# Kernel optimization log

Measured on AMD Instinct MI355X. Metric: run time of the kernel, lower is better.

## Reference

```python
import jax, jax.numpy as jnp
import numpy as np

N = 20000      # total nodes
E = 160000     # total edges
G = 64         # graphs in batch
D_ESM = 1280
D = 512
OUT = 500
NUM_LAYERS = 3


def setup_inputs() -> dict:
    key = jax.random.key(0)
    ks = jax.random.split(key, 16)
    s = 0.02
    inp = {
        "native_x": jax.random.randint(ks[0], (N,), 0, 21),
        "x": jax.random.normal(ks[1], (N, D_ESM), dtype=jnp.float32),
        "edge_index": jax.random.randint(ks[2], (2, E), 0, N),
        "batch": jnp.sort(jax.random.randint(ks[3], (N,), 0, G)),
        # parameters
        "embed_table": jax.random.normal(ks[4], (21, 96), dtype=jnp.float32) * s,
        "proj_aa_w": jax.random.normal(ks[5], (96, D), dtype=jnp.float32) * s,
        "proj_aa_b": jnp.zeros((D,), jnp.float32),
        "proj_esm_w": jax.random.normal(ks[6], (D_ESM, D), dtype=jnp.float32) * s,
        "proj_esm_b": jnp.zeros((D,), jnp.float32),
        "gcn_w": jax.random.normal(ks[7], (NUM_LAYERS, D, D), dtype=jnp.float32) * s,
        "gcn_b": jnp.zeros((NUM_LAYERS, D), jnp.float32),
        "ro1_w": jax.random.normal(ks[8], (D, 1024), dtype=jnp.float32) * s,
        "ro1_b": jnp.zeros((1024,), jnp.float32),
        "ro2_w": jax.random.normal(ks[9], (1024, OUT), dtype=jnp.float32) * s,
        "ro2_b": jnp.zeros((OUT,), jnp.float32),
        "weight1": jnp.array([0.6, 0.4], jnp.float32),
    }
    return inp


def _gcn_stack(feat, src, dst, enorm, self_norm, gcn_w, gcn_b):
    # GraphCNN: 3 GCNConv layers (PyG: sym-normalized adj with self loops),
    # residual add after the first layer.
    for i in range(NUM_LAYERS):
        hW = feat @ gcn_w[i]                                   # [N, D]
        msg = hW[src] * enorm[:, None]                          # [E, D] gather
        agg = jax.ops.segment_sum(msg, dst, num_segments=N)     # scatter-add
        agg = agg + hW * self_norm[:, None] + gcn_b[i]
        out = jax.nn.relu(agg)
        feat = out if i == 0 else feat + out
    return feat


def reference(native_x, x, edge_index, batch, embed_table,
              proj_aa_w, proj_aa_b, proj_esm_w, proj_esm_b,
              gcn_w, gcn_b, ro1_w, ro1_b, ro2_w, ro2_b, weight1):
    # embedding + projections (dropout = identity, eval mode)
    x_aa = embed_table[native_x] @ proj_aa_w + proj_aa_b        # [N, 512]
    x_esm_lin = x @ proj_esm_w + proj_esm_b                     # [N, 512]
    h = jax.nn.relu(x_aa + x_esm_lin)
    x_esm = jax.nn.relu(x_esm_lin)

    src, dst = edge_index[0], edge_index[1]
    # GCN normalization with self loops: deg over targets + 1
    deg = jax.ops.segment_sum(jnp.ones((E,), x.dtype), dst, num_segments=N) + 1.0
    dis = deg ** -0.5
    enorm = dis[src] * dis[dst]     # per-edge norm
    self_norm = dis * dis           # self-loop norm

    n1 = _gcn_stack(h, src, dst, enorm, self_norm, gcn_w, gcn_b)
    n3 = _gcn_stack(x_esm, src, dst, enorm, self_norm, gcn_w, gcn_b)

    # global max pool per graph
    g1 = jax.ops.segment_max(n1, batch, num_segments=G)          # [G, 512]
    g3 = jax.ops.segment_max(n3, batch, num_segments=G)

    g = weight1[0] * g1 + weight1[1] * g3
    y = jax.nn.sigmoid(jax.nn.relu(g @ ro1_w + ro1_b) @ ro2_w + ro2_b)
    return y
```

## Files before the change

### kernel.cpp

```cpp
#include <hip/hip_runtime.h>
#include <float.h>

#define NN 20000
#define EE 160000
#define GG 64
#define DD 512
#define NL 3
#define M2 40000
#define M2P 40064
#define M1 20000
#define M1P 20096
#define BK 64

typedef __bf16 bf16x8 __attribute__((ext_vector_type(8)));
typedef float f32x4 __attribute__((ext_vector_type(4)));
typedef unsigned int u32;
typedef unsigned short u16;
typedef u32 u32x4 __attribute__((ext_vector_type(4)));
typedef u32 u32x2 __attribute__((ext_vector_type(2)));

union FragU { u32x4 u; bf16x8 b; };

__device__ inline float blo(u32 u){ union{u32 i;float f;}x; x.i=u<<16; return x.f; }
__device__ inline float bhi(u32 u){ union{u32 i;float f;}x; x.i=u&0xFFFF0000u; return x.f; }
__device__ inline float bf2f(u16 v){ union{u32 i;float f;}x; x.i=((u32)v)<<16; return x.f; }
__device__ inline u16 f2bf(float f){ union{float f;u32 i;}x; x.f=f; u32 r=x.i+0x7FFFu+((x.i>>16)&1u); return (u16)(r>>16); }
__device__ inline u32 pack2(float a,float b){ return (u32)f2bf(a) | ((u32)f2bf(b)<<16); }

__device__ __forceinline__ void gload16(const void* g, void* lds){
  __builtin_amdgcn_global_load_lds(
    (const __attribute__((address_space(1))) void*)g,
    (__attribute__((address_space(3))) void*)lds, 16, 0, 0);
}

__global__ void k_cvt(const float* __restrict__ in, u16* __restrict__ outp){
  int t = blockIdx.x*256+threadIdx.x;
  if(t >= M1P*160) return;
  int row = t/160, gidx = t%160;
  u32x4 o;
  if(row < M1){
    const float* s = in + (size_t)row*1280 + gidx*8;
    float4 v0 = *(const float4*)s;
    float4 v1 = *(const float4*)(s+4);
    o.x=pack2(v0.x,v0.y); o.y=pack2(v0.z,v0.w);
    o.z=pack2(v1.x,v1.y); o.w=pack2(v1.z,v1.w);
  } else {
    o.x=o.y=o.z=o.w=0u;
  }
  *(u32x4*)(outp + (size_t)row*1280 + gidx*8) = o;
}

__global__ void k_transpose_cvt(const float* __restrict__ in, u16* __restrict__ outp, int R, int C){
  __shared__ float t[32][33];
  int c0 = blockIdx.x*32, r0 = blockIdx.y*32;
  t[threadIdx.y][threadIdx.x] = in[(size_t)(r0+threadIdx.y)*C + c0+threadIdx.x];
  __syncthreads();
  outp[(size_t)(c0+threadIdx.y)*R + r0+threadIdx.x] = f2bf(t[threadIdx.x][threadIdx.y]);
}

__global__ void k_transpose_f32(const float* __restrict__ in, float* __restrict__ outp, int R, int C){
  __shared__ float t[32][33];
  int c0 = blockIdx.x*32, r0 = blockIdx.y*32;
  int r = r0+threadIdx.y, c = c0+threadIdx.x;
  if(r<R && c<C) t[threadIdx.y][threadIdx.x] = in[(size_t)r*C + c];
  __syncthreads();
  int oc = c0+threadIdx.y, orr = r0+threadIdx.x;
  if(oc<C && orr<R) outp[(size_t)oc*R + orr] = t[threadIdx.x][threadIdx.y];
}

__global__ void k_embp(const float* __restrict__ et, const float* __restrict__ w,
                       const float* __restrict__ b, float* __restrict__ outp){
  int t = blockIdx.x*256+threadIdx.x;
  if(t >= 21*512) return;
  int a = t>>9, d = t&511;
  float s = b[d];
  for(int k=0;k<96;k++) s += et[a*96+k]*w[k*512+d];
  outp[t] = s;
}

__global__ void k_deg(const int* __restrict__ ei, int* __restrict__ deg){
  int e = blockIdx.x*256+threadIdx.x; if(e>=EE) return;
  atomicAdd(&deg[ei[EE+e]], 1);
}
__global__ void k_dis(const int* __restrict__ deg, float* __restrict__ dis){
  int n = blockIdx.x*256+threadIdx.x; if(n>=NN) return;
  dis[n] = rsqrtf((float)deg[n] + 1.0f);
}
__global__ void k_scan(const int* __restrict__ deg, int* __restrict__ offs){
  __shared__ int part[1024];
  int tid = threadIdx.x;
  int base = tid*20;
  int s=0;
  for(int i=0;i<20;i++){ int idx=base+i; if(idx<NN) s += deg[idx]; }
  part[tid]=s; __syncthreads();
  for(int off=1; off<1024; off<<=1){
    int v = (tid>=off)? part[tid-off] : 0;
    __syncthreads();
    part[tid] += v;
    __syncthreads();
  }
  int pre = (tid>0)? part[tid-1] : 0;
  for(int i=0;i<20;i++){ int idx=base+i; if(idx<NN){ offs[idx]=pre; pre += deg[idx]; } }
  if(tid==1023) offs[NN]=part[1023];
}
__global__ void k_fill(const int* __restrict__ ei, const int* __restrict__ offs, int* __restrict__ curs,
                       const float* __restrict__ dis, int* __restrict__ csrs, float* __restrict__ csrw){
  int e = blockIdx.x*256+threadIdx.x; if(e>=EE) return;
  int s = ei[e], d = ei[EE+e];
  int pos = atomicAdd(&curs[d],1);
  int slot = offs[d]+pos;
  csrs[slot]=s;
  csrw[slot]=dis[s]*dis[d];
}

__global__ __launch_bounds__(256) void k_gemm(const u16* __restrict__ A, const u16* __restrict__ Bt,
                                              u16* __restrict__ C, int Mstore, int K, int lda){
  __shared__ u16 lsA[128*BK];
  __shared__ u16 lsB[128*BK];
  const int tid = threadIdx.x;
  const int lane = tid & 63;
  const int wid = tid >> 6;
  const int wr = wid >> 1, wc = wid & 1;
  const int la = lane & 15, lg = lane >> 4;
  const int n0 = blockIdx.x * 128;
  const int rowB = blockIdx.y * 128;

  f32x4 acc[4][4];
  #pragma unroll
  for(int m=0;m<4;m++)
    #pragma unroll
    for(int n=0;n<4;n++)
      #pragma unroll
      for(int r=0;r<4;r++) acc[m][n][r]=0.f;

  const u16* Arow = A + (size_t)rowB*lda;
  const u16* Brow = Bt + (size_t)n0*K;

  int srow[4], scol[4], ldsoff[4];
  #pragma unroll
  for(int i=0;i<4;i++){
    int li = i*256+tid;
    srow[i] = li>>3;
    scol[i] = ((li&7) ^ (srow[i]&7))*8;
    ldsoff[i] = (i*256 + wid*64)*8;
  }

  for(int k0=0;k0<K;k0+=BK){
    #pragma unroll
    for(int i=0;i<4;i++)
      gload16(Arow + (size_t)srow[i]*lda + k0 + scol[i], lsA + ldsoff[i]);
    #pragma unroll
    for(int i=0;i<4;i++)
      gload16(Brow + (size_t)srow[i]*K + k0 + scol[i], lsB + ldsoff[i]);
    __syncthreads();
    #pragma unroll
    for(int kk=0;kk<2;kk++){
      FragU aF[4], bF[4];
      #pragma unroll
      for(int m=0;m<4;m++){
        int row = wr*64+m*16+la;
        aF[m].u = *(const u32x4*)&lsA[row*BK + ((kk*4+lg)^(row&7))*8];
      }
      #pragma unroll
      for(int n=0;n<4;n++){
        int row = wc*64+n*16+la;
        bF[n].u = *(const u32x4*)&lsB[row*BK + ((kk*4+lg)^(row&7))*8];
      }
      #pragma unroll
      for(int m=0;m<4;m++)
        #pragma unroll
        for(int n=0;n<4;n++)
          acc[m][n] = __builtin_amdgcn_mfma_f32_16x16x32_bf16(aF[m].b, bF[n].b, acc[m][n], 0,0,0);
    }
    __syncthreads();
  }
  #pragma unroll
  for(int m=0;m<4;m++)
    #pragma unroll
    for(int n=0;n<4;n++)
      #pragma unroll
      for(int r=0;r<4;r++){
        int rr = rowB + wr*64 + m*16 + lg*4 + r;
        if(rr < Mstore)
          C[(size_t)rr*512 + n0 + wc*64 + n*16 + la] = f2bf(acc[m][n][r]);
      }
}

__global__ void k_fuse(const u16* __restrict__ xW, const int* __restrict__ nx,
                       const float* __restrict__ embp, const float* __restrict__ esm_b,
                       u16* __restrict__ feat){
  int t = blockIdx.x*256+threadIdx.x;
  if(t >= NN*64) return;
  int n = t>>6, c = (t&63)*8;
  uint4 q = *(const uint4*)(xW + (size_t)n*512 + c);
  int a = nx[n];
  float xw[8] = {blo(q.x),bhi(q.x),blo(q.y),bhi(q.y),blo(q.z),bhi(q.z),blo(q.w),bhi(q.w)};
  float h[8], ee[8];
  #pragma unroll
  for(int j=0;j<8;j++){
    float t1 = xw[j] + esm_b[c+j];
    float hh = embp[a*512 + c + j] + t1;
    h[j]  = hh>0.f?hh:0.f;
    ee[j] = t1>0.f?t1:0.f;
  }
  uint4 o1, o2;
  o1.x=pack2(h[0],h[1]); o1.y=pack2(h[2],h[3]); o1.z=pack2(h[4],h[5]); o1.w=pack2(h[6],h[7]);
  o2.x=pack2(ee[0],ee[1]); o2.y=pack2(ee[2],ee[3]); o2.z=pack2(ee[4],ee[5]); o2.w=pack2(ee[6],ee[7]);
  *(uint4*)(feat + (size_t)n*512 + c) = o1;
  *(uint4*)(feat + (size_t)(n+NN)*512 + c) = o2;
}

__global__ __launch_bounds__(64) void k_agg(const u16* __restrict__ hW, u16* __restrict__ feat,
                 const int* __restrict__ offs, const int* __restrict__ csrs,
                 const float* __restrict__ csrw, const float* __restrict__ dis,
                 const float* __restrict__ bias, int layer){
  const int v = blockIdx.x;
  const int lane = threadIdx.x;
  const int nn  = (v < NN) ? v : v - NN;
  const int soff = (v < NN) ? 0 : NN;
  const int e0 = offs[nn], e1 = offs[nn+1];
  float acc[8] = {0,0,0,0,0,0,0,0};
  for(int e=e0;e<e1;++e){
    int s = csrs[e] + soff;
    float wgt = csrw[e];
    uint4 q = *(const uint4*)(hW + (size_t)s*512 + lane*8);
    acc[0]+=wgt*blo(q.x); acc[1]+=wgt*bhi(q.x);
    acc[2]+=wgt*blo(q.y); acc[3]+=wgt*bhi(q.y);
    acc[4]+=wgt*blo(q.z); acc[5]+=wgt*bhi(q.z);
    acc[6]+=wgt*blo(q.w); acc[7]+=wgt*bhi(q.w);
  }
  float dn = dis[nn]; float sn = dn*dn;
  uint4 qs = *(const uint4*)(hW + (size_t)v*512 + lane*8);
  acc[0]+=sn*blo(qs.x); acc[1]+=sn*bhi(qs.x); acc[2]+=sn*blo(qs.y); acc[3]+=sn*bhi(qs.y);
  acc[4]+=sn*blo(qs.z); acc[5]+=sn*bhi(qs.z); acc[6]+=sn*blo(qs.w); acc[7]+=sn*bhi(qs.w);
  float4 b0 = *(const float4*)(bias + lane*8);
  float4 b1 = *(const float4*)(bias + lane*8 + 4);
  acc[0]+=b0.x; acc[1]+=b0.y; acc[2]+=b0.z; acc[3]+=b0.w;
  acc[4]+=b1.x; acc[5]+=b1.y; acc[6]+=b1.z; acc[7]+=b1.w;
  #pragma unroll
  for(int j=0;j<8;j++) acc[j] = acc[j]>0.f ? acc[j] : 0.f;
  if(layer>0){
    uint4 qf = *(const uint4*)(feat + (size_t)v*512 + lane*8);
    acc[0]+=blo(qf.x); acc[1]+=bhi(qf.x); acc[2]+=blo(qf.y); acc[3]+=bhi(qf.y);
    acc[4]+=blo(qf.z); acc[5]+=bhi(qf.z); acc[6]+=blo(qf.w); acc[7]+=bhi(qf.w);
  }
  uint4 o;
  o.x=pack2(acc[0],acc[1]); o.y=pack2(acc[2],acc[3]);
  o.z=pack2(acc[4],acc[5]); o.w=pack2(acc[6],acc[7]);
  *(uint4*)(feat + (size_t)v*512 + lane*8) = o;
}

__global__ void k_bounds(const int* __restrict__ batch, int* __restrict__ starts){
  int n = blockIdx.x*256+threadIdx.x;
  if(n>=NN) return;
  int b = batch[n];
  int pb = n ? batch[n-1] : -1;
  for(int g=pb+1; g<=b; g++) starts[g]=n;
  if(n==NN-1){ for(int g=b+1; g<=GG; g++) starts[g]=NN; }
}

__global__ void k_pool(const u16* __restrict__ feat, const int* __restrict__ starts,
                       u32* __restrict__ m1, u32* __restrict__ m3){
  int g = blockIdx.x, c = blockIdx.y;
  int s = starts[g], e = starts[g+1];
  int len = e - s;
  int b0 = s + (len*c)/8, b1 = s + (len*(c+1))/8;
  int t = threadIdx.x;
  float a0=0.f, a1=0.f, c0=0.f, c1=0.f;
  for(int n=b0;n<b1;++n){
    u32 q1 = *(const u32*)(feat + (size_t)n*512 + t*2);
    u32 q3 = *(const u32*)(feat + (size_t)(n+NN)*512 + t*2);
    a0 = fmaxf(a0, blo(q1)); a1 = fmaxf(a1, bhi(q1));
    c0 = fmaxf(c0, blo(q3)); c1 = fmaxf(c1, bhi(q3));
  }
  atomicMax(m1 + g*512 + t*2,     __float_as_uint(a0));
  atomicMax(m1 + g*512 + t*2 + 1, __float_as_uint(a1));
  atomicMax(m3 + g*512 + t*2,     __float_as_uint(c0));
  atomicMax(m3 + g*512 + t*2 + 1, __float_as_uint(c1));
}
__global__ void k_gcomb(const u32* __restrict__ m1, const u32* __restrict__ m3,
                        const float* __restrict__ w1, float* __restrict__ gc){
  int t = blockIdx.x*256+threadIdx.x; if(t>=GG*512) return;
  gc[t] = w1[0]*__uint_as_float(m1[t]) + w1[1]*__uint_as_float(m3[t]);
}

__global__ __launch_bounds__(256) void k_ro1v(const float* __restrict__ gc, const float* __restrict__ wT,
                                              const float* __restrict__ b, float* __restrict__ r1){
  int gw = blockIdx.x*4 + (threadIdx.x>>6);
  int g = gw >> 10, o = gw & 1023;
  int lane = threadIdx.x & 63;
  const float4* gr = (const float4*)(gc + (size_t)g*512);
  const float4* wr = (const float4*)(wT + (size_t)o*512);
  float s = 0.f;
  #pragma unroll
  for(int i=0;i<2;i++){
    float4 a = gr[i*64+lane];
    float4 w = wr[i*64+lane];
    s += a.x*w.x + a.y*w.y + a.z*w.z + a.w*w.w;
  }
  #pragma unroll
  for(int m=32;m>=1;m>>=1) s += __shfl_xor(s, m, 64);
  if(lane==0){ s += b[o]; r1[gw] = s>0.f ? s : 0.f; }
}
__global__ __launch_bounds__(256) void k_ro2v(const float* __restrict__ r1, const float* __restrict__ wT,
                                              const float* __restrict__ b, float* __restrict__ y){
  int gw = blockIdx.x*4 + (threadIdx.x>>6);
  int g = gw/500, o = gw - g*500;
  int lane = threadIdx.x & 63;
  const float4* gr = (const float4*)(r1 + (size_t)g*1024);
  const float4* wr = (const float4*)(wT + (size_t)o*1024);
  float s = 0.f;
  #pragma unroll
  for(int i=0;i<4;i++){
    float4 a = gr[i*64+lane];
    float4 w = wr[i*64+lane];
    s += a.x*w.x + a.y*w.y + a.z*w.z + a.w*w.w;
  }
  #pragma unroll
  for(int m=32;m>=1;m>>=1) s += __shfl_xor(s, m, 64);
  if(lane==0) y[gw] = 1.0f/(1.0f+__expf(-(s + b[o])));
}

extern "C" void kernel_launch(void* const* d_in, const int* in_sizes, int n_in,
                              void* d_out, int out_size, void* d_ws, size_t ws_size,
                              hipStream_t stream){
  const int*   native_x = (const int*)d_in[0];
  const float* x        = (const float*)d_in[1];
  const int*   ei       = (const int*)d_in[2];
  const int*   batch    = (const int*)d_in[3];
  const float* embed_t  = (const float*)d_in[4];
  const float* paa_w    = (const float*)d_in[5];
  const float* paa_b    = (const float*)d_in[6];
  const float* pesm_w   = (const float*)d_in[7];
  const float* pesm_b   = (const float*)d_in[8];
  const float* gcn_w    = (const float*)d_in[9];
  const float* gcn_b    = (const float*)d_in[10];
  const float* ro1_w    = (const float*)d_in[11];
  const float* ro1_b    = (const float*)d_in[12];
  const float* ro2_w    = (const float*)d_in[13];
  const float* ro2_b    = (const float*)d_in[14];
  const float* w1       = (const float*)d_in[15];
  float* out = (float*)d_out;

  char* p = (char*)d_ws;
  auto alloc = [&](size_t n){ void* r = (void*)p; p += (n + 255) & ~(size_t)255; return r; };
  u16* feat   = (u16*)alloc((size_t)M2P*512*2);
  u16* hW     = (u16*)alloc((size_t)M2P*512*2);
  u16* xbf    = (u16*)alloc((size_t)M1P*1280*2);
  u16* WtE    = (u16*)alloc((size_t)512*1280*2);
  u16* WtG    = (u16*)alloc((size_t)3*512*512*2);
  float* roT1 = (float*)alloc((size_t)1024*512*4);
  float* roT2 = (float*)alloc((size_t)500*1024*4);
  float* embp = (float*)alloc(21*512*4);
  int* deg    = (int*)alloc(NN*4);
  float* dis  = (float*)alloc(NN*4);
  int* offs   = (int*)alloc((NN+1)*4);
  int* curs   = (int*)alloc(NN*4);
  int* csrs   = (int*)alloc(EE*4);
  float* csrw = (float*)alloc(EE*4);
  int* starts = (int*)alloc((GG+1)*4);
  u32* m1b    = (u32*)alloc(GG*512*4);
  u32* m3b    = (u32*)alloc(GG*512*4);
  float* gc   = (float*)alloc(GG*512*4);
  float* r1   = (float*)alloc(GG*1024*4);
  (void)ws_size; (void)in_sizes; (void)n_in; (void)out_size;

  hipMemsetAsync(deg,  0, NN*4, stream);
  hipMemsetAsync(curs, 0, NN*4, stream);
  hipMemsetAsync(m1b,  0, GG*512*4, stream);
  hipMemsetAsync(m3b,  0, GG*512*4, stream);

  k_cvt<<<(M1P*160+255)/256,256,0,stream>>>(x, xbf);
  k_transpose_cvt<<<dim3(16,40),dim3(32,32),0,stream>>>(pesm_w, WtE, 1280, 512);
  for(int i=0;i<3;i++)
    k_transpose_cvt<<<dim3(16,16),dim3(32,32),0,stream>>>(gcn_w+(size_t)i*262144, WtG+(size_t)i*262144, 512, 512);
  k_transpose_f32<<<dim3(32,16),dim3(32,32),0,stream>>>(ro1_w, roT1, 512, 1024);
  k_transpose_f32<<<dim3(16,32),dim3(32,32),0,stream>>>(ro2_w, roT2, 1024, 500);
  k_embp<<<42,256,0,stream>>>(embed_t, paa_w, paa_b, embp);
  k_deg<<<(EE+255)/256,256,0,stream>>>(ei, deg);
  k_dis<<<(NN+255)/256,256,0,stream>>>(deg, dis);
  k_scan<<<1,1024,0,stream>>>(deg, offs);
  k_fill<<<(EE+255)/256,256,0,stream>>>(ei, offs, curs, dis, csrs, csrw);

  k_gemm<<<dim3(4,157),256,0,stream>>>(xbf, WtE, hW, M1, 1280, 1280);
  k_fuse<<<(NN*64+255)/256,256,0,stream>>>(hW, native_x, embp, pesm_b, feat);

  for(int i=0;i<3;i++){
    k_gemm<<<dim3(4,313),256,0,stream>>>(feat, WtG+(size_t)i*262144, hW, M2, 512, 512);
    k_agg<<<M2,64,0,stream>>>(hW, feat, offs, csrs, csrw, dis, gcn_b+(size_t)i*512, i);
  }

  k_bounds<<<(NN+255)/256,256,0,stream>>>(batch, starts);
  k_pool<<<dim3(GG,8),256,0,stream>>>(feat, starts, m1b, m3b);
  k_gcomb<<<(GG*512+255)/256,256,0,stream>>>(m1b, m3b, w1, gc);
  k_ro1v<<<16384,256,0,stream>>>(gc, roT1, ro1_b, r1);
  k_ro2v<<<8000,256,0,stream>>>(r1, roT2, ro2_b, out);
}
```

Baseline: 481.7 us.

## Interleave the two GCN stacks row-wise and split aggregation across edge-parallel lanes

Node features for the two GCN stacks are stored interleaved, as rows 2n and 2n+1, instead of as two separate halves. A neighbour gather therefore fetches both stacks' rows for a source node from adjacent memory, and the CSR index and weight are shared between the two streams. The aggregation kernel becomes a 256-thread block in which each wave handles one node and a 64-column slice, with 4 lane groups walking edges in parallel and combining through cross-lane shuffles. The aim is to shorten the serial, latency-bound per-edge loop and raise memory-level parallelism. The cost is redundant edge-metadata loads across the 8 column slices and the shuffle-reduction overhead.

```diff
diff --git a/kernel.cpp b/kernel.cpp
--- a/kernel.cpp
+++ b/kernel.cpp
@@ -31,6 +31,13 @@
   __builtin_amdgcn_global_load_lds(
     (const __attribute__((address_space(1))) void*)g,
     (__attribute__((address_space(3))) void*)lds, 16, 0, 0);
+}
+
+__device__ __forceinline__ void acc8(float* a, uint4 q, float w){
+  a[0]+=w*blo(q.x); a[1]+=w*bhi(q.x);
+  a[2]+=w*blo(q.y); a[3]+=w*bhi(q.y);
+  a[4]+=w*blo(q.z); a[5]+=w*bhi(q.z);
+  a[6]+=w*blo(q.w); a[7]+=w*bhi(q.w);
 }
 
 __global__ void k_cvt(const float* __restrict__ in, u16* __restrict__ outp){
@@ -206,48 +213,64 @@
   uint4 o1, o2;
   o1.x=pack2(h[0],h[1]); o1.y=pack2(h[2],h[3]); o1.z=pack2(h[4],h[5]); o1.w=pack2(h[6],h[7]);
   o2.x=pack2(ee[0],ee[1]); o2.y=pack2(ee[2],ee[3]); o2.z=pack2(ee[4],ee[5]); o2.w=pack2(ee[6],ee[7]);
-  *(uint4*)(feat + (size_t)n*512 + c) = o1;
-  *(uint4*)(feat + (size_t)(n+NN)*512 + c) = o2;
-}
-
-__global__ __launch_bounds__(64) void k_agg(const u16* __restrict__ hW, u16* __restrict__ feat,
+  *(uint4*)(feat + (size_t)(2*n)*512 + c) = o1;
+  *(uint4*)(feat + (size_t)(2*n+1)*512 + c) = o2;
+}
+
+__global__ __launch_bounds__(256) void k_agg3(const u16* __restrict__ hW, u16* __restrict__ feat,
                  const int* __restrict__ offs, const int* __restrict__ csrs,
                  const float* __restrict__ csrw, const float* __restrict__ dis,
                  const float* __restrict__ bias, int layer){
-  const int v = blockIdx.x;
-  const int lane = threadIdx.x;
-  const int nn  = (v < NN) ? v : v - NN;
-  const int soff = (v < NN) ? 0 : NN;
+  const int tid = threadIdx.x;
+  const int wv = tid >> 6;
+  const int lane = tid & 63;
+  const int slice = blockIdx.x & 7;
+  const int nn = ((blockIdx.x >> 3) << 2) + wv;
+  const int g = lane >> 4;
+  const int p = lane & 15;
+  const int st = p >> 3;
+  const int ch = p & 7;
+  const int eo = slice*64 + ch*8;
+
   const int e0 = offs[nn], e1 = offs[nn+1];
   float acc[8] = {0,0,0,0,0,0,0,0};
-  for(int e=e0;e<e1;++e){
-    int s = csrs[e] + soff;
-    float wgt = csrw[e];
-    uint4 q = *(const uint4*)(hW + (size_t)s*512 + lane*8);
-    acc[0]+=wgt*blo(q.x); acc[1]+=wgt*bhi(q.x);
-    acc[2]+=wgt*blo(q.y); acc[3]+=wgt*bhi(q.y);
-    acc[4]+=wgt*blo(q.z); acc[5]+=wgt*bhi(q.z);
-    acc[6]+=wgt*blo(q.w); acc[7]+=wgt*bhi(q.w);
-  }
-  float dn = dis[nn]; float sn = dn*dn;
-  uint4 qs = *(const uint4*)(hW + (size_t)v*512 + lane*8);
-  acc[0]+=sn*blo(qs.x); acc[1]+=sn*bhi(qs.x); acc[2]+=sn*blo(qs.y); acc[3]+=sn*bhi(qs.y);
-  acc[4]+=sn*blo(qs.z); acc[5]+=sn*bhi(qs.z); acc[6]+=sn*blo(qs.w); acc[7]+=sn*bhi(qs.w);
-  float4 b0 = *(const float4*)(bias + lane*8);
-  float4 b1 = *(const float4*)(bias + lane*8 + 4);
+
+  uint4 qs = *(const uint4*)(hW + (size_t)(2*nn+st)*512 + eo);
+  float dn = dis[nn], sn = dn*dn;
+
+  for(int eb = e0; eb < e1; eb += 4){
+    int e = eb + g;
+    uint4 q = make_uint4(0u,0u,0u,0u);
+    float wgt = 0.f;
+    if(e < e1){
+      int s = csrs[e];
+      wgt = csrw[e];
+      q = *(const uint4*)(hW + (size_t)(2*s+st)*512 + eo);
+    }
+    acc8(acc, q, wgt);
+  }
+  #pragma unroll
+  for(int j=0;j<8;j++){
+    acc[j] += __shfl_xor(acc[j], 16, 64);
+    acc[j] += __shfl_xor(acc[j], 32, 64);
+  }
+  acc8(acc, qs, sn);
+  float4 b0 = *(const float4*)(bias + eo);
+  float4 b1 = *(const float4*)(bias + eo + 4);
   acc[0]+=b0.x; acc[1]+=b0.y; acc[2]+=b0.z; acc[3]+=b0.w;
   acc[4]+=b1.x; acc[5]+=b1.y; acc[6]+=b1.z; acc[7]+=b1.w;
   #pragma unroll
   for(int j=0;j<8;j++) acc[j] = acc[j]>0.f ? acc[j] : 0.f;
   if(layer>0){
-    uint4 qf = *(const uint4*)(feat + (size_t)v*512 + lane*8);
-    acc[0]+=blo(qf.x); acc[1]+=bhi(qf.x); acc[2]+=blo(qf.y); acc[3]+=bhi(qf.y);
-    acc[4]+=blo(qf.z); acc[5]+=bhi(qf.z); acc[6]+=blo(qf.w); acc[7]+=bhi(qf.w);
-  }
-  uint4 o;
-  o.x=pack2(acc[0],acc[1]); o.y=pack2(acc[2],acc[3]);
-  o.z=pack2(acc[4],acc[5]); o.w=pack2(acc[6],acc[7]);
-  *(uint4*)(feat + (size_t)v*512 + lane*8) = o;
+    uint4 qf = *(const uint4*)(feat + (size_t)(2*nn+st)*512 + eo);
+    acc8(acc, qf, 1.f);
+  }
+  if(g==0){
+    uint4 o;
+    o.x=pack2(acc[0],acc[1]); o.y=pack2(acc[2],acc[3]);
+    o.z=pack2(acc[4],acc[5]); o.w=pack2(acc[6],acc[7]);
+    *(uint4*)(feat + (size_t)(2*nn+st)*512 + eo) = o;
+  }
 }
 
 __global__ void k_bounds(const int* __restrict__ batch, int* __restrict__ starts){
@@ -268,8 +291,9 @@
   int t = threadIdx.x;
   float a0=0.f, a1=0.f, c0=0.f, c1=0.f;
   for(int n=b0;n<b1;++n){
-    u32 q1 = *(const u32*)(feat + (size_t)n*512 + t*2);
-    u32 q3 = *(const u32*)(feat + (size_t)(n+NN)*512 + t*2);
+    const u16* pr = feat + (size_t)(2*n)*512 + t*2;
+    u32 q1 = *(const u32*)pr;
+    u32 q3 = *(const u32*)(pr + 512);
     a0 = fmaxf(a0, blo(q1)); a1 = fmaxf(a1, bhi(q1));
     c0 = fmaxf(c0, blo(q3)); c1 = fmaxf(c1, bhi(q3));
   }
@@ -387,7 +411,7 @@
 
   for(int i=0;i<3;i++){
     k_gemm<<<dim3(4,313),256,0,stream>>>(feat, WtG+(size_t)i*262144, hW, M2, 512, 512);
-    k_agg<<<M2,64,0,stream>>>(hW, feat, offs, csrs, csrw, dis, gcn_b+(size_t)i*512, i);
+    k_agg3<<<NN*2,256,0,stream>>>(hW, feat, offs, csrs, csrw, dis, gcn_b+(size_t)i*512, i);
   }
 
   k_bounds<<<(NN+255)/256,256,0,stream>>>(batch, starts);
```

New measurement: 521.8 us. +8.3%, slower.
